# Performance work log

Hardware: AMD Instinct MI355X
Metric: run time of the kernel (lower is better)

The kernel has to match this reference:

```python
import jax, jax.numpy as jnp
import numpy as np

NEG_INF = -1e9


def setup_inputs() -> dict:
    key = jax.random.key(0)
    ks = jax.random.split(key, 6)
    B, S, D, H, Dh = 2, 2048, 1024, 16, 64
    scale = 1.0 / np.sqrt(D)
    return {
        "x": jax.random.normal(ks[0], (B, S, D), jnp.float32),
        "W_Q": jax.random.normal(ks[1], (H, D, Dh), jnp.float32) * scale,
        "b_Q": jnp.zeros((H, Dh), jnp.float32),
        "W_K": jax.random.normal(ks[2], (H, D, Dh), jnp.float32) * scale,
        "b_K": jnp.zeros((H, Dh), jnp.float32),
        "W_V": jax.random.normal(ks[3], (H, D, Dh), jnp.float32) * scale,
        "W_O": jax.random.normal(ks[4], (H, Dh, D), jnp.float32) * scale,
        "b_V": jnp.zeros((H, Dh), jnp.float32),
        "b_O": jnp.zeros((H, D), jnp.float32),
    }


def reference(x, W_Q, b_Q, W_K, b_K, W_V, W_O, b_V, b_O):
    # x: [b, s, m]; W_{Q,K,V}: [h, m, d]; W_O: [h, d, m]
    S = x.shape[1]
    d_head = W_Q.shape[-1]

    q = jnp.einsum("bqm,hmd->bqhd", x, W_Q) + b_Q  # [b, q, h, d]
    k = jnp.einsum("bkm,hmd->bkhd", x, W_K) + b_K
    v = jnp.einsum("bkm,hmd->bkhd", x, W_V) + b_V

    scores = jnp.einsum("bqhd,bkhd->bhqk", q, k) / jnp.sqrt(
        jnp.asarray(d_head, x.dtype)
    )  # [b, h, q, k] -- full score matrix, as in the unfused original
    causal = jnp.tril(jnp.ones((S, S), bool))
    scores = jnp.where(causal, scores, jnp.asarray(NEG_INF, x.dtype))
    attn = jax.nn.softmax(scores, axis=-1)

    z = jnp.einsum("bhqk,bkhd->bqhd", attn, v)  # [b, q, h, d]
    # per-head output proj then sum over heads; b_O is [h, m] per the annotation
    out = jnp.einsum("bqhd,hdm->bqm", z, W_O) + jnp.sum(b_O, axis=0)
    return out
```

## Files before the change

### kernel.cpp

```cpp
#include <hip/hip_runtime.h>
#include <cstdint>

typedef unsigned short u16;
typedef short s8v __attribute__((ext_vector_type(8)));
typedef float f4v __attribute__((ext_vector_type(4)));

__device__ __forceinline__ u16 f2b(float f) {
  uint32_t u = __float_as_uint(f);
  u = (u + 0x7FFFu + ((u >> 16) & 1u)) >> 16;
  return (u16)u;
}

__device__ __forceinline__ uint32_t pk2(float a, float b) {
  uint32_t r;
  asm("v_cvt_pk_bf16_f32 %0, %1, %2" : "=v"(r) : "v"(a), "v"(b));
  return r;
}

__device__ __forceinline__ void gload16(const u16* g, u16* l) {
  __builtin_amdgcn_global_load_lds(
      (const __attribute__((address_space(1))) void*)g,
      (__attribute__((address_space(3))) void*)l, 16, 0, 0);
}

__global__ void prep(const float* __restrict__ x, u16* __restrict__ xb,
                     const float* __restrict__ WQ, const float* __restrict__ WK,
                     const float* __restrict__ WV, const float* __restrict__ WO,
                     u16* __restrict__ WTqkv, u16* __restrict__ WOT,
                     const float* __restrict__ bQ, const float* __restrict__ bK,
                     const float* __restrict__ bV, const float* __restrict__ bO,
                     float* __restrict__ bqkv, float* __restrict__ bsum) {
  __shared__ u16 tile[64][65];
  const int bid = blockIdx.x;
  const int tid = threadIdx.x;

  if (bid < 4096) {
    int i = bid * 256 + tid;
    float4 v = ((const float4*)x)[i];
    uint2 o;
    o.x = (uint32_t)f2b(v.x) | ((uint32_t)f2b(v.y) << 16);
    o.y = (uint32_t)f2b(v.z) | ((uint32_t)f2b(v.w) << 16);
    ((uint2*)xb)[i] = o;
  } else if (bid < 4864) {
    int sub = bid - 4096;
    int w = sub >> 8, sub2 = sub & 255;
    const float* W = (w == 0) ? WQ : (w == 1) ? WK : WV;
    u16* dst = WTqkv + (size_t)w * 1024 * 1024;
    const int m0 = (sub2 & 15) * 64;
    const int h  = sub2 >> 4;
    const int c  = tid & 63;
    const int r4 = tid >> 6;
    const float* Wh = W + (size_t)h * 65536;
    for (int i = 0; i < 16; ++i) {
      int lm = i * 4 + r4;
      tile[lm][c] = f2b(Wh[(size_t)(m0 + lm) * 64 + c]);
    }
    __syncthreads();
    for (int i = 0; i < 16; ++i) {
      int dd = i * 4 + r4;
      dst[((size_t)h * 64 + dd) * 1024 + m0 + c] = tile[c][dd];
    }
  } else if (bid < 5120) {
    int sub = bid - 4864;
    const int k0 = (sub & 15) * 64;
    const int m0 = (sub >> 4) * 64;
    const int c  = tid & 63;
    const int r4 = tid >> 6;
    for (int i = 0; i < 16; ++i) {
      int lk = i * 4 + r4;
      tile[lk][c] = f2b(WO[(size_t)(k0 + lk) * 1024 + m0 + c]);
    }
    __syncthreads();
    for (int i = 0; i < 16; ++i) {
      int lm = i * 4 + r4;
      WOT[(size_t)(m0 + lm) * 1024 + k0 + c] = tile[c][lm];
    }
  } else {
    int t = (bid - 5120) * 256 + tid;
    if (t < 1024)       bqkv[t] = bQ[t];
    else if (t < 2048)  bqkv[t] = bK[t - 1024];
    else if (t < 3072)  bqkv[t] = bV[t - 2048];
    else {
      int m = t - 3072;
      float s = 0.f;
      for (int hh = 0; hh < 16; ++hh) s += bO[hh * 1024 + m];
      bsum[m] = s;
    }
  }
}

__global__ void convT_v(const u16* __restrict__ QKV, u16* __restrict__ VT) {
  __shared__ u16 tile[64][65];
  const int r0 = blockIdx.x * 64;
  const int c0 = blockIdx.y * 64;
  const int c  = threadIdx.x & 63;
  const int r4 = threadIdx.x >> 6;
  for (int i = 0; i < 16; ++i) {
    int lr = i * 4 + r4;
    tile[lr][c] = QKV[(size_t)(r0 + lr) * 3072 + 2048 + c0 + c];
  }
  __syncthreads();
  for (int i = 0; i < 16; ++i) {
    int lc = i * 4 + r4;
    VT[(size_t)(c0 + lc) * 4096 + r0 + c] = tile[c][lc];
  }
}

template<bool OUT_F32>
__global__ void gemm_bt(const u16* __restrict__ A, const u16* __restrict__ BT,
                        const float* __restrict__ bias, void* __restrict__ Cout,
                        int N, int K, int scale_cols) {
  __shared__ __align__(16) u16 sA[128 * 32];
  __shared__ __align__(16) u16 sB[128 * 32];
  const int tid  = threadIdx.x;
  const int lane = tid & 63, wave = tid >> 6;
  const int wm = wave >> 1, wn = wave & 1;
  const int lq = lane & 15, quad = lane >> 4;
  const int m0 = blockIdx.y * 128, n0 = blockIdx.x * 128;

  f4v acc[4][4] = {};

  for (int k0 = 0; k0 < K; k0 += 32) {
    __syncthreads();
    for (int i = 0; i < 2; ++i) {
      int s = tid + i * 256;
      int row = s >> 2, part = s & 3;
      gload16(A  + (size_t)(m0 + row) * K + k0 + part * 8, &sA[s * 8]);
      gload16(BT + (size_t)(n0 + row) * K + k0 + part * 8, &sB[s * 8]);
    }
    __syncthreads();
    s8v af[4], bfr[4];
    for (int i = 0; i < 4; ++i)
      af[i]  = *(const s8v*)&sA[(wm * 64 + i * 16 + lq) * 32 + quad * 8];
    for (int j = 0; j < 4; ++j)
      bfr[j] = *(const s8v*)&sB[(wn * 64 + j * 16 + lq) * 32 + quad * 8];
    for (int i = 0; i < 4; ++i)
      for (int j = 0; j < 4; ++j)
        acc[i][j] = __builtin_amdgcn_mfma_f32_16x16x32_bf16(af[i], bfr[j], acc[i][j], 0, 0, 0);
  }

  for (int i = 0; i < 4; ++i)
    for (int j = 0; j < 4; ++j) {
      int row = m0 + wm * 64 + i * 16 + quad * 4;
      int col = n0 + wn * 64 + j * 16 + lq;
      float bb = bias[col];
      float sc = (col < scale_cols) ? 0.125f : 1.0f;
      for (int r = 0; r < 4; ++r) {
        float v = (acc[i][j][r] + bb) * sc;
        if (OUT_F32) ((float*)Cout)[(size_t)(row + r) * N + col] = v;
        else         ((u16*)Cout)[(size_t)(row + r) * N + col] = f2b(v);
      }
    }
}

__global__ __launch_bounds__(64, 2) void attn_fwd(const u16* __restrict__ QKV,
                                                  const u16* __restrict__ VT,
                                                  u16* __restrict__ Z) {
  __shared__ __align__(16) u16 sP[2][2][16 * 72];
  const int lane = threadIdx.x;
  const int lq = lane & 15, quad = lane >> 4;

  const int id   = blockIdx.x;
  const int xcd  = id & 7;
  const int slot = id >> 3;
  const int g    = xcd + 8 * (slot >> 6);
  const int s    = slot & 63;
  const int u    = (s < 32) ? (63 - s) : (s - 32);
  const int h = g & 15, b = g >> 4;
  const int qA = u * 32, qB = qA + 16;
  const int nchunk = u / 2 + 1;

  const int RS = 3072;
  const u16* base = QKV + (size_t)b * 2048 * RS;
  const u16* Qb  = base + h * 64;
  const u16* Kb  = base + 1024 + h * 64;
  const u16* VTb = VT + (size_t)h * 64 * 4096 + (size_t)b * 2048;

  s8v qfA0 = *(const s8v*)&Qb[(size_t)(qA + lq) * RS + quad * 8];
  s8v qfA1 = *(const s8v*)&Qb[(size_t)(qA + lq) * RS + 32 + quad * 8];
  s8v qfB0 = *(const s8v*)&Qb[(size_t)(qB + lq) * RS + quad * 8];
  s8v qfB1 = *(const s8v*)&Qb[(size_t)(qB + lq) * RS + 32 + quad * 8];

  f4v zA[4] = {}, zB[4] = {};
  float mA = -3.0e38f, lA = 0.f, mB = -3.0e38f, lB = 0.f;

  s8v kf[8], vf[8];

#define LOADK(c_) do {                                                        \
    const int kk0_ = (c_) * 64;                                               \
    _Pragma("unroll")                                                         \
    for (int i_ = 0; i_ < 4; ++i_) {                                          \
      const u16* kr_ = &Kb[(size_t)(kk0_ + 16 * i_ + lq) * RS + quad * 8];    \
      kf[2 * i_]     = *(const s8v*)kr_;                                      \
      kf[2 * i_ + 1] = *(const s8v*)(kr_ + 32);                               \
    }                                                                         \
  } while (0)

#define LOADV(c_) do {                                                        \
    const int kk0_ = (c_) * 64;                                               \
    _Pragma("unroll")                                                         \
    for (int d_ = 0; d_ < 4; ++d_) {                                          \
      const u16* vr_ = &VTb[(size_t)(d_ * 16 + lq) * 4096 + kk0_ + quad * 8]; \
      vf[d_]     = *(const s8v*)vr_;                                          \
      vf[d_ + 4] = *(const s8v*)(vr_ + 32);                                   \
    }                                                                         \
  } while (0)

  auto SMW = [&](int c, int qt0, float& mrow, float& lsum, f4v (&zacc)[4],
                 u16* sPt, f4v (&sc)[4]) {
    float sv[4][4];
    for (int i = 0; i < 4; ++i)
      for (int r = 0; r < 4; ++r) sv[i][r] = sc[i][r];
    if (c + 1 == nchunk) {
      const int kb = c * 64;
      for (int i = 0; i < 4; ++i)
        for (int r = 0; r < 4; ++r)
          if (kb + 16 * i + quad * 4 + r > qt0 + lq) sv[i][r] = -3.0e38f;
    }
    float lmax = sv[0][0];
    for (int i = 0; i < 4; ++i)
      for (int r = 0; r < 4; ++r) lmax = fmaxf(lmax, sv[i][r]);
    if (!__all(lmax <= mrow + 8.0f)) {
      float t = lmax;
      t = fmaxf(t, __shfl_xor(t, 16, 64));
      t = fmaxf(t, __shfl_xor(t, 32, 64));
      float mnew = fmaxf(mrow, t);
      float al = __expf(mrow - mnew);
      mrow = mnew;
      lsum *= al;
      float alr[4];
      for (int r = 0; r < 4; ++r) alr[r] = __shfl(al, quad * 4 + r, 16);
      for (int dc = 0; dc < 4; ++dc)
        for (int r = 0; r < 4; ++r) zacc[dc][r] *= alr[r];
    }
    float acc = 0.f;
    float p[4][4];
    for (int i = 0; i < 4; ++i)
      for (int r = 0; r < 4; ++r) {
        p[i][r] = __expf(sv[i][r] - mrow);
        acc += p[i][r];
      }
    lsum += acc;
    for (int i = 0; i < 4; ++i) {
      uint2 w;
      w.x = pk2(p[i][0], p[i][1]);
      w.y = pk2(p[i][2], p[i][3]);
      *(uint2*)&sPt[lq * 72 + 16 * i + quad * 4] = w;
    }
  };

#define QK(aA_, aB_) do {                                                     \
    _Pragma("unroll")                                                         \
    for (int i_ = 0; i_ < 4; ++i_) {                                          \
      aA_[i_] = __builtin_amdgcn_mfma_f32_16x16x32_bf16(kf[2*i_],   qfA0, aA_[i_], 0, 0, 0); \
      aA_[i_] = __builtin_amdgcn_mfma_f32_16x16x32_bf16(kf[2*i_+1], qfA1, aA_[i_], 0, 0, 0); \
      aB_[i_] = __builtin_amdgcn_mfma_f32_16x16x32_bf16(kf[2*i_],   qfB0, aB_[i_], 0, 0, 0); \
      aB_[i_] = __builtin_amdgcn_mfma_f32_16x16x32_bf16(kf[2*i_+1], qfB1, aB_[i_], 0, 0, 0); \
    }                                                                         \
  } while (0)

  auto PV = [&](int pb) {
    s8v pA0 = *(const s8v*)&sP[0][pb][lq * 72 + quad * 8];
    s8v pA1 = *(const s8v*)&sP[0][pb][lq * 72 + 32 + quad * 8];
    s8v pB0 = *(const s8v*)&sP[1][pb][lq * 72 + quad * 8];
    s8v pB1 = *(const s8v*)&sP[1][pb][lq * 72 + 32 + quad * 8];
#pragma unroll
    for (int d_ = 0; d_ < 4; ++d_) {
      zA[d_] = __builtin_amdgcn_mfma_f32_16x16x32_bf16(pA0, vf[d_],     zA[d_], 0, 0, 0);
      zA[d_] = __builtin_amdgcn_mfma_f32_16x16x32_bf16(pA1, vf[d_ + 4], zA[d_], 0, 0, 0);
      zB[d_] = __builtin_amdgcn_mfma_f32_16x16x32_bf16(pB0, vf[d_],     zB[d_], 0, 0, 0);
      zB[d_] = __builtin_amdgcn_mfma_f32_16x16x32_bf16(pB1, vf[d_ + 4], zB[d_], 0, 0, 0);
    }
  };

  LOADK(0);
  {
    f4v aA[4] = {}, aB[4] = {};
    __builtin_amdgcn_s_setprio(1);
    QK(aA, aB);
    __builtin_amdgcn_s_setprio(0);
    if (nchunk > 1) LOADK(1);
    LOADV(0);
    SMW(0, qA, mA, lA, zA, sP[0][0], aA);
    SMW(0, qB, mB, lB, zB, sP[1][0], aB);
    asm volatile("" ::: "memory");
  }

  for (int c = 1; c < nchunk; ++c) {
    f4v aA[4] = {}, aB[4] = {};
    __builtin_amdgcn_s_setprio(1);
    QK(aA, aB);
    PV((c + 1) & 1);
    __builtin_amdgcn_s_setprio(0);
    asm volatile("" ::: "memory");
    if (c + 1 < nchunk) LOADK(c + 1);
    LOADV(c);
    SMW(c, qA, mA, lA, zA, sP[0][c & 1], aA);
    SMW(c, qB, mB, lB, zB, sP[1][c & 1], aB);
    asm volatile("" ::: "memory");
  }

  {
    __builtin_amdgcn_s_setprio(1);
    PV((nchunk - 1) & 1);
    __builtin_amdgcn_s_setprio(0);
  }
#undef QK
#undef LOADK
#undef LOADV

  lA += __shfl_xor(lA, 16, 64); lA += __shfl_xor(lA, 32, 64);
  lB += __shfl_xor(lB, 16, 64); lB += __shfl_xor(lB, 32, 64);
  float invA[4], invB[4];
  for (int r = 0; r < 4; ++r) {
    invA[r] = 1.0f / __shfl(lA, quad * 4 + r, 16);
    invB[r] = 1.0f / __shfl(lB, quad * 4 + r, 16);
  }
  for (int dc = 0; dc < 4; ++dc)
    for (int r = 0; r < 4; ++r) {
      size_t rowA = (size_t)b * 2048 + qA + quad * 4 + r;
      size_t rowB = (size_t)b * 2048 + qB + quad * 4 + r;
      Z[rowA * 1024 + h * 64 + dc * 16 + lq] = f2b(zA[dc][r] * invA[r]);
      Z[rowB * 1024 + h * 64 + dc * 16 + lq] = f2b(zB[dc][r] * invB[r]);
    }
}

extern "C" void kernel_launch(void* const* d_in, const int* in_sizes, int n_in,
                              void* d_out, int out_size, void* d_ws, size_t ws_size,
                              hipStream_t stream) {
  const float* x  = (const float*)d_in[0];
  const float* WQ = (const float*)d_in[1];
  const float* bQ = (const float*)d_in[2];
  const float* WK = (const float*)d_in[3];
  const float* bK = (const float*)d_in[4];
  const float* WV = (const float*)d_in[5];
  const float* WO = (const float*)d_in[6];
  const float* bV = (const float*)d_in[7];
  const float* bO = (const float*)d_in[8];
  float* out = (float*)d_out;

  uint8_t* ws = (uint8_t*)d_ws;
  u16*   xb    = (u16*)(ws);
  u16*   VTv   = (u16*)(ws);
  u16*   WTqkv = (u16*)(ws + 8388608);
  u16*   WOT   = (u16*)(ws + 14680064);
  u16*   QKV   = (u16*)(ws + 16777216);
  u16*   Zb    = (u16*)(ws + 41943040);
  float* bqkv  = (float*)(ws + 50331648);
  float* bsum  = (float*)(ws + 50343936);

  prep<<<5136, 256, 0, stream>>>(x, xb, WQ, WK, WV, WO, WTqkv, WOT,
                                 bQ, bK, bV, bO, bqkv, bsum);
  gemm_bt<false><<<dim3(24, 32), 256, 0, stream>>>(xb, WTqkv, bqkv, (void*)QKV, 3072, 1024, 1024);
  convT_v<<<dim3(64, 16), 256, 0, stream>>>(QKV, VTv);
  attn_fwd<<<dim3(2048, 1, 1), 64, 0, stream>>>(QKV, VTv, Zb);
  gemm_bt<true><<<dim3(8, 32), 256, 0, stream>>>(Zb, WOT, bsum, (void*)out, 1024, 1024, 0);
}
```

Before: 223.1 us.

## Split long causal attention rows across two blocks, double-buffer GEMM LDS

The attention kernel now splits the query tiles in the second half of each sequence (those with the most key chunks) into two blocks that each handle half the key range. Each half writes unnormalized fp32 partial outputs and (max, sum) stats, and a new combine kernel merges them into the bf16 Z. This is meant to balance work across blocks under causal masking. The GEMM gains double-buffered LDS staging with one barrier per k-step, and the output projection uses a 128x64 tile, giving 512 blocks instead of 256. Attention launch bounds rise to 4 waves per SIMD. The split path runs only if the workspace is large enough, and it adds an extra launch plus fp32 partial-buffer traffic.

```diff
diff --git a/kernel.cpp b/kernel.cpp
--- a/kernel.cpp
+++ b/kernel.cpp
@@ -106,43 +106,60 @@
   }
 }
 
-template<bool OUT_F32>
+template<bool OUT_F32, int BN>
 __global__ void gemm_bt(const u16* __restrict__ A, const u16* __restrict__ BT,
                         const float* __restrict__ bias, void* __restrict__ Cout,
                         int N, int K, int scale_cols) {
-  __shared__ __align__(16) u16 sA[128 * 32];
-  __shared__ __align__(16) u16 sB[128 * 32];
+  __shared__ __align__(16) u16 sA[2][128 * 32];
+  __shared__ __align__(16) u16 sB[2][BN * 32];
   const int tid  = threadIdx.x;
   const int lane = tid & 63, wave = tid >> 6;
   const int wm = wave >> 1, wn = wave & 1;
   const int lq = lane & 15, quad = lane >> 4;
-  const int m0 = blockIdx.y * 128, n0 = blockIdx.x * 128;
-
-  f4v acc[4][4] = {};
-
-  for (int k0 = 0; k0 < K; k0 += 32) {
-    __syncthreads();
+  const int m0 = blockIdx.y * 128, n0 = blockIdx.x * BN;
+  constexpr int NJ = BN / 32;
+
+  f4v acc[4][NJ] = {};
+
+  auto STAGE = [&](int buf, int k0) {
     for (int i = 0; i < 2; ++i) {
       int s = tid + i * 256;
       int row = s >> 2, part = s & 3;
-      gload16(A  + (size_t)(m0 + row) * K + k0 + part * 8, &sA[s * 8]);
-      gload16(BT + (size_t)(n0 + row) * K + k0 + part * 8, &sB[s * 8]);
-    }
+      gload16(A + (size_t)(m0 + row) * K + k0 + part * 8, &sA[buf][s * 8]);
+    }
+    if (BN == 128) {
+      for (int i = 0; i < 2; ++i) {
+        int s = tid + i * 256;
+        int row = s >> 2, part = s & 3;
+        gload16(BT + (size_t)(n0 + row) * K + k0 + part * 8, &sB[buf][s * 8]);
+      }
+    } else {
+      int row = tid >> 2, part = tid & 3;
+      gload16(BT + (size_t)(n0 + row) * K + k0 + part * 8, &sB[buf][tid * 8]);
+    }
+  };
+
+  STAGE(0, 0);
+  __syncthreads();
+  int cur = 0;
+  for (int k0 = 0; k0 < K; k0 += 32) {
+    if (k0 + 32 < K) STAGE(cur ^ 1, k0 + 32);
+    s8v af[4], bfr[NJ];
+    for (int i = 0; i < 4; ++i)
+      af[i]  = *(const s8v*)&sA[cur][(wm * 64 + i * 16 + lq) * 32 + quad * 8];
+    for (int j = 0; j < NJ; ++j)
+      bfr[j] = *(const s8v*)&sB[cur][(wn * (BN / 2) + j * 16 + lq) * 32 + quad * 8];
+    for (int i = 0; i < 4; ++i)
+      for (int j = 0; j < NJ; ++j)
+        acc[i][j] = __builtin_amdgcn_mfma_f32_16x16x32_bf16(af[i], bfr[j], acc[i][j], 0, 0, 0);
     __syncthreads();
-    s8v af[4], bfr[4];
-    for (int i = 0; i < 4; ++i)
-      af[i]  = *(const s8v*)&sA[(wm * 64 + i * 16 + lq) * 32 + quad * 8];
-    for (int j = 0; j < 4; ++j)
-      bfr[j] = *(const s8v*)&sB[(wn * 64 + j * 16 + lq) * 32 + quad * 8];
-    for (int i = 0; i < 4; ++i)
-      for (int j = 0; j < 4; ++j)
-        acc[i][j] = __builtin_amdgcn_mfma_f32_16x16x32_bf16(af[i], bfr[j], acc[i][j], 0, 0, 0);
+    cur ^= 1;
   }
 
   for (int i = 0; i < 4; ++i)
-    for (int j = 0; j < 4; ++j) {
+    for (int j = 0; j < NJ; ++j) {
       int row = m0 + wm * 64 + i * 16 + quad * 4;
-      int col = n0 + wn * 64 + j * 16 + lq;
+      int col = n0 + wn * (BN / 2) + j * 16 + lq;
       float bb = bias[col];
       float sc = (col < scale_cols) ? 0.125f : 1.0f;
       for (int r = 0; r < 4; ++r) {
@@ -153,22 +170,44 @@
     }
 }
 
-__global__ __launch_bounds__(64, 2) void attn_fwd(const u16* __restrict__ QKV,
+template<bool SPLIT>
+__global__ __launch_bounds__(64, 4) void attn_fwd(const u16* __restrict__ QKV,
                                                   const u16* __restrict__ VT,
-                                                  u16* __restrict__ Z) {
+                                                  u16* __restrict__ Z,
+                                                  float* __restrict__ Zp,
+                                                  float2* __restrict__ ml) {
   __shared__ __align__(16) u16 sP[2][2][16 * 72];
   const int lane = threadIdx.x;
   const int lq = lane & 15, quad = lane >> 4;
 
-  const int id   = blockIdx.x;
-  const int xcd  = id & 7;
-  const int slot = id >> 3;
-  const int g    = xcd + 8 * (slot >> 6);
-  const int s    = slot & 63;
-  const int u    = (s < 32) ? (63 - s) : (s - 32);
+  int g, u, c_lo, c_hi, part_p;
+  const int id  = blockIdx.x;
+  const int xcd = id & 7;
+  if (SPLIT) {
+    const int slot = id >> 3;
+    const int cwx  = slot / 96;
+    const int rr   = slot % 96;
+    const int s0   = rr & 31;
+    const int role = rr >> 5;
+    g = xcd + 8 * cwx;
+    if (role == 0) { u = s0; c_lo = 0; c_hi = u / 2 + 1; part_p = -1; }
+    else {
+      u = 63 - s0;
+      const int nc = u / 2 + 1, nc0 = nc >> 1;
+      part_p = role - 1;
+      c_lo = part_p ? nc0 : 0;
+      c_hi = part_p ? nc  : nc0;
+    }
+  } else {
+    const int slot = id >> 3;
+    g = xcd + 8 * (slot >> 6);
+    const int ss = slot & 63;
+    u = (ss < 32) ? (63 - ss) : (ss - 32);
+    c_lo = 0; c_hi = u / 2 + 1; part_p = -1;
+  }
+  const int nfull = u / 2 + 1;
   const int h = g & 15, b = g >> 4;
   const int qA = u * 32, qB = qA + 16;
-  const int nchunk = u / 2 + 1;
 
   const int RS = 3072;
   const u16* base = QKV + (size_t)b * 2048 * RS;
@@ -211,7 +250,7 @@
     float sv[4][4];
     for (int i = 0; i < 4; ++i)
       for (int r = 0; r < 4; ++r) sv[i][r] = sc[i][r];
-    if (c + 1 == nchunk) {
+    if (c == nfull - 1) {
       const int kb = c * 64;
       for (int i = 0; i < 4; ++i)
         for (int r = 0; r < 4; ++r)
@@ -273,27 +312,27 @@
     }
   };
 
-  LOADK(0);
+  LOADK(c_lo);
   {
     f4v aA[4] = {}, aB[4] = {};
     __builtin_amdgcn_s_setprio(1);
     QK(aA, aB);
     __builtin_amdgcn_s_setprio(0);
-    if (nchunk > 1) LOADK(1);
-    LOADV(0);
-    SMW(0, qA, mA, lA, zA, sP[0][0], aA);
-    SMW(0, qB, mB, lB, zB, sP[1][0], aB);
+    if (c_lo + 1 < c_hi) LOADK(c_lo + 1);
+    LOADV(c_lo);
+    SMW(c_lo, qA, mA, lA, zA, sP[0][c_lo & 1], aA);
+    SMW(c_lo, qB, mB, lB, zB, sP[1][c_lo & 1], aB);
     asm volatile("" ::: "memory");
   }
 
-  for (int c = 1; c < nchunk; ++c) {
+  for (int c = c_lo + 1; c < c_hi; ++c) {
     f4v aA[4] = {}, aB[4] = {};
     __builtin_amdgcn_s_setprio(1);
     QK(aA, aB);
     PV((c + 1) & 1);
     __builtin_amdgcn_s_setprio(0);
     asm volatile("" ::: "memory");
-    if (c + 1 < nchunk) LOADK(c + 1);
+    if (c + 1 < c_hi) LOADK(c + 1);
     LOADV(c);
     SMW(c, qA, mA, lA, zA, sP[0][c & 1], aA);
     SMW(c, qB, mB, lB, zB, sP[1][c & 1], aB);
@@ -302,7 +341,7 @@
 
   {
     __builtin_amdgcn_s_setprio(1);
-    PV((nchunk - 1) & 1);
+    PV((c_hi - 1) & 1);
     __builtin_amdgcn_s_setprio(0);
   }
 #undef QK
@@ -311,18 +350,59 @@
 
   lA += __shfl_xor(lA, 16, 64); lA += __shfl_xor(lA, 32, 64);
   lB += __shfl_xor(lB, 16, 64); lB += __shfl_xor(lB, 32, 64);
-  float invA[4], invB[4];
-  for (int r = 0; r < 4; ++r) {
-    invA[r] = 1.0f / __shfl(lA, quad * 4 + r, 16);
-    invB[r] = 1.0f / __shfl(lB, quad * 4 + r, 16);
-  }
-  for (int dc = 0; dc < 4; ++dc)
+
+  if (!SPLIT || part_p < 0) {
+    float invA[4], invB[4];
     for (int r = 0; r < 4; ++r) {
-      size_t rowA = (size_t)b * 2048 + qA + quad * 4 + r;
-      size_t rowB = (size_t)b * 2048 + qB + quad * 4 + r;
-      Z[rowA * 1024 + h * 64 + dc * 16 + lq] = f2b(zA[dc][r] * invA[r]);
-      Z[rowB * 1024 + h * 64 + dc * 16 + lq] = f2b(zB[dc][r] * invB[r]);
-    }
+      invA[r] = 1.0f / __shfl(lA, quad * 4 + r, 16);
+      invB[r] = 1.0f / __shfl(lB, quad * 4 + r, 16);
+    }
+    for (int dc = 0; dc < 4; ++dc)
+      for (int r = 0; r < 4; ++r) {
+        size_t rowA = (size_t)b * 2048 + qA + quad * 4 + r;
+        size_t rowB = (size_t)b * 2048 + qB + quad * 4 + r;
+        Z[rowA * 1024 + h * 64 + dc * 16 + lq] = f2b(zA[dc][r] * invA[r]);
+        Z[rowB * 1024 + h * 64 + dc * 16 + lq] = f2b(zB[dc][r] * invB[r]);
+      }
+  } else {
+    float* ZpP = Zp + (size_t)part_p * (32768 * 64);
+    const int prA = g * 1024 + (qA - 1024) + quad * 4;
+    const int prB = g * 1024 + (qB - 1024) + quad * 4;
+    for (int dc = 0; dc < 4; ++dc)
+      for (int r = 0; r < 4; ++r) {
+        ZpP[(size_t)(prA + r) * 64 + dc * 16 + lq] = zA[dc][r];
+        ZpP[(size_t)(prB + r) * 64 + dc * 16 + lq] = zB[dc][r];
+      }
+    if (quad == 0) {
+      ml[(size_t)part_p * 32768 + g * 1024 + (qA - 1024) + lq] = make_float2(mA, lA);
+      ml[(size_t)part_p * 32768 + g * 1024 + (qB - 1024) + lq] = make_float2(mB, lB);
+    }
+  }
+}
+
+__global__ void combine(const float* __restrict__ Zp, const float2* __restrict__ ml,
+                        u16* __restrict__ Z) {
+  const int t = blockIdx.x * 256 + threadIdx.x;
+  const int row = t >> 4;
+  const int dseg = (t & 15) * 4;
+  const float2 a = ml[row];
+  const float2 c = ml[32768 + row];
+  const float M  = fmaxf(a.x, c.x);
+  const float w0 = __expf(a.x - M), w1 = __expf(c.x - M);
+  const float inv = 1.0f / (a.y * w0 + c.y * w1);
+  const float4 z0 = *(const float4*)&Zp[(size_t)row * 64 + dseg];
+  const float4 z1 = *(const float4*)&Zp[(size_t)32768 * 64 + (size_t)row * 64 + dseg];
+  const float o0 = (z0.x * w0 + z1.x * w1) * inv;
+  const float o1 = (z0.y * w0 + z1.y * w1) * inv;
+  const float o2 = (z0.z * w0 + z1.z * w1) * inv;
+  const float o3 = (z0.w * w0 + z1.w * w1) * inv;
+  const int g = row >> 10, qloc = row & 1023;
+  const int bb = g >> 4, hh = g & 15;
+  const size_t zoff = ((size_t)bb * 2048 + 1024 + qloc) * 1024 + hh * 64 + dseg;
+  uint2 w;
+  w.x = pk2(o0, o1);
+  w.y = pk2(o2, o3);
+  *(uint2*)&Z[zoff] = w;
 }
 
 extern "C" void kernel_launch(void* const* d_in, const int* in_sizes, int n_in,
@@ -348,11 +428,19 @@
   u16*   Zb    = (u16*)(ws + 41943040);
   float* bqkv  = (float*)(ws + 50331648);
   float* bsum  = (float*)(ws + 50343936);
+  float* Zp    = (float*)(ws + 50348032);
+  float2* mlp  = (float2*)(ws + 67125248);
+  const bool do_split = ws_size >= 67649536ull;
 
   prep<<<5136, 256, 0, stream>>>(x, xb, WQ, WK, WV, WO, WTqkv, WOT,
                                  bQ, bK, bV, bO, bqkv, bsum);
-  gemm_bt<false><<<dim3(24, 32), 256, 0, stream>>>(xb, WTqkv, bqkv, (void*)QKV, 3072, 1024, 1024);
+  gemm_bt<false, 128><<<dim3(24, 32), 256, 0, stream>>>(xb, WTqkv, bqkv, (void*)QKV, 3072, 1024, 1024);
   convT_v<<<dim3(64, 16), 256, 0, stream>>>(QKV, VTv);
-  attn_fwd<<<dim3(2048, 1, 1), 64, 0, stream>>>(QKV, VTv, Zb);
-  gemm_bt<true><<<dim3(8, 32), 256, 0, stream>>>(Zb, WOT, bsum, (void*)out, 1024, 1024, 0);
-}
+  if (do_split) {
+    attn_fwd<true><<<dim3(3072, 1, 1), 64, 0, stream>>>(QKV, VTv, Zb, Zp, mlp);
+    combine<<<2048, 256, 0, stream>>>(Zp, mlp, Zb);
+  } else {
+    attn_fwd<false><<<dim3(2048, 1, 1), 64, 0, stream>>>(QKV, VTv, Zb, Zp, mlp);
+  }
+  gemm_bt<true, 64><<<dim3(16, 32), 256, 0, stream>>>(Zb, WOT, bsum, (void*)out, 1024, 1024, 0);
+}
```

New measurement: 330.9 us. 1.48x slower.

## Double-buffer GEMM LDS staging and retile QKV and output projections

Applied to the files above, without the earlier changes.

Templates the bf16 GEMM on tile sizes and thread count and adds double-buffered LDS staging, so the next K-slice's global-to-LDS loads are issued before computing on the current slice. This replaces the two barriers per iteration with one and lets loads overlap MFMA work. The QKV projection now uses 256x128 tiles with 512 threads, and the output projection uses 128x64 tiles so it launches more blocks. The cost is twice the LDS per block and a different occupancy and grid shape for each GEMM.

```diff
diff --git a/kernel.cpp b/kernel.cpp
--- a/kernel.cpp
+++ b/kernel.cpp
@@ -106,43 +106,60 @@
   }
 }
 
-template<bool OUT_F32>
+template<bool OUT_F32, int BM, int BN, int NTHR>
 __global__ void gemm_bt(const u16* __restrict__ A, const u16* __restrict__ BT,
                         const float* __restrict__ bias, void* __restrict__ Cout,
                         int N, int K, int scale_cols) {
-  __shared__ __align__(16) u16 sA[128 * 32];
-  __shared__ __align__(16) u16 sB[128 * 32];
+  constexpr int NW = NTHR / 64;
+  constexpr int WM = NW / 2;
+  constexpr int NJ = BN / 32;
+  static_assert(BM / WM == 64, "per-wave rows must be 64");
+  static_assert(BM * 4 == 2 * NTHR, "A staging: 2 segs/thread");
+  static_assert(BN * 4 == NTHR, "B staging: 1 seg/thread");
+
+  __shared__ __align__(16) u16 sA[2][BM * 32];
+  __shared__ __align__(16) u16 sB[2][BN * 32];
   const int tid  = threadIdx.x;
   const int lane = tid & 63, wave = tid >> 6;
   const int wm = wave >> 1, wn = wave & 1;
   const int lq = lane & 15, quad = lane >> 4;
-  const int m0 = blockIdx.y * 128, n0 = blockIdx.x * 128;
-
-  f4v acc[4][4] = {};
-
+  const int m0 = blockIdx.y * BM, n0 = blockIdx.x * BN;
+
+  f4v acc[4][NJ] = {};
+
+  auto STAGE = [&](int buf, int k0) {
+    for (int i = 0; i < 2; ++i) {
+      int s = tid + i * NTHR;
+      int row = s >> 2, part = s & 3;
+      gload16(A + (size_t)(m0 + row) * K + k0 + part * 8, &sA[buf][s * 8]);
+    }
+    {
+      int row = tid >> 2, part = tid & 3;
+      gload16(BT + (size_t)(n0 + row) * K + k0 + part * 8, &sB[buf][tid * 8]);
+    }
+  };
+
+  STAGE(0, 0);
+  __syncthreads();
+  int cur = 0;
   for (int k0 = 0; k0 < K; k0 += 32) {
+    if (k0 + 32 < K) STAGE(cur ^ 1, k0 + 32);
+    s8v af[4], bfr[NJ];
+    for (int i = 0; i < 4; ++i)
+      af[i]  = *(const s8v*)&sA[cur][(wm * 64 + i * 16 + lq) * 32 + quad * 8];
+    for (int j = 0; j < NJ; ++j)
+      bfr[j] = *(const s8v*)&sB[cur][(wn * (BN / 2) + j * 16 + lq) * 32 + quad * 8];
+    for (int i = 0; i < 4; ++i)
+      for (int j = 0; j < NJ; ++j)
+        acc[i][j] = __builtin_amdgcn_mfma_f32_16x16x32_bf16(af[i], bfr[j], acc[i][j], 0, 0, 0);
     __syncthreads();
-    for (int i = 0; i < 2; ++i) {
-      int s = tid + i * 256;
-      int row = s >> 2, part = s & 3;
-      gload16(A  + (size_t)(m0 + row) * K + k0 + part * 8, &sA[s * 8]);
-      gload16(BT + (size_t)(n0 + row) * K + k0 + part * 8, &sB[s * 8]);
-    }
-    __syncthreads();
-    s8v af[4], bfr[4];
-    for (int i = 0; i < 4; ++i)
-      af[i]  = *(const s8v*)&sA[(wm * 64 + i * 16 + lq) * 32 + quad * 8];
-    for (int j = 0; j < 4; ++j)
-      bfr[j] = *(const s8v*)&sB[(wn * 64 + j * 16 + lq) * 32 + quad * 8];
-    for (int i = 0; i < 4; ++i)
-      for (int j = 0; j < 4; ++j)
-        acc[i][j] = __builtin_amdgcn_mfma_f32_16x16x32_bf16(af[i], bfr[j], acc[i][j], 0, 0, 0);
+    cur ^= 1;
   }
 
   for (int i = 0; i < 4; ++i)
-    for (int j = 0; j < 4; ++j) {
+    for (int j = 0; j < NJ; ++j) {
       int row = m0 + wm * 64 + i * 16 + quad * 4;
-      int col = n0 + wn * 64 + j * 16 + lq;
+      int col = n0 + wn * (BN / 2) + j * 16 + lq;
       float bb = bias[col];
       float sc = (col < scale_cols) ? 0.125f : 1.0f;
       for (int r = 0; r < 4; ++r) {
@@ -351,8 +368,10 @@
 
   prep<<<5136, 256, 0, stream>>>(x, xb, WQ, WK, WV, WO, WTqkv, WOT,
                                  bQ, bK, bV, bO, bqkv, bsum);
-  gemm_bt<false><<<dim3(24, 32), 256, 0, stream>>>(xb, WTqkv, bqkv, (void*)QKV, 3072, 1024, 1024);
+  gemm_bt<false, 256, 128, 512><<<dim3(24, 16), 512, 0, stream>>>(
+      xb, WTqkv, bqkv, (void*)QKV, 3072, 1024, 1024);
   convT_v<<<dim3(64, 16), 256, 0, stream>>>(QKV, VTv);
   attn_fwd<<<dim3(2048, 1, 1), 64, 0, stream>>>(QKV, VTv, Zb);
-  gemm_bt<true><<<dim3(8, 32), 256, 0, stream>>>(Zb, WOT, bsum, (void*)out, 1024, 1024, 0);
-}
+  gemm_bt<true, 128, 64, 256><<<dim3(16, 32), 256, 0, stream>>>(
+      Zb, WOT, bsum, (void*)out, 1024, 1024, 0);
+}
```

New measurement: 220.7 us. About the same (-1.1%).
